# Performance work log

Hardware: AMD Instinct MI355X
Metric: run time of the kernel (lower is better)

## Reference

```python
import jax
import jax.numpy as jnp
from jax import lax
import numpy as np

DIM = 256
WIN = 7


def setup_inputs() -> dict:
    key = jax.random.key(0)
    ks = jax.random.split(key, 7)
    B, C, H, W = 16, DIM, 64, 64
    k = WIN
    return {
        "x": jax.random.normal(ks[0], (B, C, H, W), dtype=jnp.float32),
        "dw_weight": jax.random.normal(ks[1], (C, 1, k, k), dtype=jnp.float32) * 0.1,
        "pw_weight": jax.random.normal(ks[2], (C, C), dtype=jnp.float32) * 0.05,
        "w1": jax.random.normal(ks[3], (C // 4, C), dtype=jnp.float32) * 0.05,
        "b1": jax.random.normal(ks[4], (C // 4,), dtype=jnp.float32) * 0.05,
        "w2": jax.random.normal(ks[5], (C * k * k, C // 4), dtype=jnp.float32) * 0.05,
        "b2": jax.random.normal(ks[6], (C * k * k,), dtype=jnp.float32) * 0.05,
    }


def reference(x, dw_weight, pw_weight, w1, b1, w2, b2):
    B, C, H, W = x.shape
    k = dw_weight.shape[-1]
    pad = k // 2
    # dynamic kernel generator: global avg pool -> 1x1 conv -> GELU -> 1x1 conv
    pooled = x.mean(axis=(2, 3))                                  # [B, C]
    h = jax.nn.gelu(pooled @ w1.T + b1, approximate=False)        # [B, C//4]
    dyn = (h @ w2.T + b2).reshape(B, C, 1, k, k)                  # [B, C, 1, k, k]
    # fuse static depthwise weights with dynamic per-sample weights
    fused = dw_weight[None] + dyn                                  # [B, C, 1, k, k]
    # per-instance depthwise conv via groups = B*C
    x_flat = x.reshape(1, B * C, H, W)
    kern = fused.reshape(B * C, 1, k, k)
    out = lax.conv_general_dilated(
        x_flat, kern,
        window_strides=(1, 1),
        padding=[(pad, pad), (pad, pad)],
        feature_group_count=B * C,
        dimension_numbers=("NCHW", "OIHW", "NCHW"),
    )
    out = out.reshape(B, C, H, W)
    # final 1x1 pointwise conv (no bias)
    return jnp.einsum("bchw,oc->bohw", out, pw_weight)
```

## Files before the change

### kernel.cpp

```cpp
#include <hip/hip_runtime.h>
#include <math.h>
#include <stdint.h>

typedef __attribute__((ext_vector_type(8))) short short8;
typedef __attribute__((ext_vector_type(4))) float f32x4;

#define B_  16
#define C_  256
#define HW_ 4096
#define KK_ 49
#define CR_ 64

__device__ __forceinline__ ushort f2bf(float f) {
    union { float f; uint32_t u; } v; v.f = f;
    uint32_t r = (v.u + 0x7FFFu + ((v.u >> 16) & 1u)) >> 16;
    return (ushort)r;
}

__global__ __launch_bounds__(256) void pool_kernel(const float* __restrict__ x,
                                                   float* __restrict__ pooled) {
    int bc = blockIdx.x;
    const float4* p4 = (const float4*)(x + (size_t)bc * HW_);
    float s = 0.f;
    for (int i = threadIdx.x; i < HW_ / 4; i += 256) {
        float4 v = p4[i];
        s += (v.x + v.y) + (v.z + v.w);
    }
#pragma unroll
    for (int off = 32; off > 0; off >>= 1) s += __shfl_down(s, off);
    __shared__ float red[4];
    if ((threadIdx.x & 63) == 0) red[threadIdx.x >> 6] = s;
    __syncthreads();
    if (threadIdx.x == 0)
        pooled[bc] = (red[0] + red[1] + red[2] + red[3]) * (1.f / HW_);
}

__global__ __launch_bounds__(64) void mlp_kernel(const float* __restrict__ pooled,
                                                 const float* __restrict__ w1,
                                                 const float* __restrict__ b1,
                                                 float* __restrict__ h) {
    int b = blockIdx.x;
    int r = threadIdx.x;
    __shared__ float pr[C_];
    for (int i = r; i < C_; i += 64) pr[i] = pooled[b * C_ + i];
    __syncthreads();
    float acc = b1[r];
    const float* wr = w1 + (size_t)r * C_;
    for (int c = 0; c < C_; c += 4) {
        float4 wv = *(const float4*)(wr + c);
        acc += pr[c] * wv.x + pr[c + 1] * wv.y + pr[c + 2] * wv.z + pr[c + 3] * wv.w;
    }
    h[b * CR_ + r] = 0.5f * acc * (1.f + erff(acc * 0.70710678118654752f));
}

__global__ __launch_bounds__(256) void genw_kernel(const float* __restrict__ h,
                                                   const float* __restrict__ w2,
                                                   const float* __restrict__ b2,
                                                   const float* __restrict__ dw,
                                                   float* __restrict__ fused) {
    __shared__ float hs[B_ * CR_];
    int m = blockIdx.x * 256 + threadIdx.x;
    for (int i = threadIdx.x; i < B_ * CR_; i += 256) hs[i] = h[i];
    float wrow[CR_];
    const float4* w4 = (const float4*)(w2 + (size_t)m * CR_);
#pragma unroll
    for (int i = 0; i < CR_ / 4; i++) {
        float4 v = w4[i];
        wrow[4 * i] = v.x; wrow[4 * i + 1] = v.y;
        wrow[4 * i + 2] = v.z; wrow[4 * i + 3] = v.w;
    }
    float base = b2[m] + dw[m];
    __syncthreads();
    for (int b = 0; b < B_; b++) {
        float acc = base;
        const float* hb = hs + b * CR_;
#pragma unroll
        for (int r = 0; r < CR_; r++) acc += hb[r] * wrow[r];
        fused[(size_t)b * (C_ * KK_) + m] = acc;
    }
}

__global__ __launch_bounds__(256) void prep_kernel(const float* __restrict__ pw,
                                                   ushort* __restrict__ Pa) {
    int idx = blockIdx.x * 256 + threadIdx.x;
    int o = idx >> 8, c = idx & 255;
    Pa[(size_t)(((o >> 4) * 32) + (c >> 3)) * 128 + (o & 15) * 8 + (c & 7)] = f2bf(pw[idx]);
}

__global__ __launch_bounds__(512, 4) void dw_kernel(const float* __restrict__ x,
                                                    const float* __restrict__ fused,
                                                    ushort* __restrict__ Ug) {
    __shared__ __align__(16) float xs[8 * 22 * 72];
    ushort* Us = (ushort*)xs;

    const int strip = blockIdx.x;
    const int cb    = blockIdx.y;
    const int b     = blockIdx.z;
    const int tid   = threadIdx.x;
    const int wid   = tid >> 6;
    const int lane  = tid & 63;
    const int c0    = cb * 8;
    const int r0    = strip * 16;

    {
        const float* xp = x + (((size_t)(b * C_ + c0 + wid)) << 12);
        float* xd = xs + wid * 1584;
#pragma unroll
        for (int row = 0; row < 22; row++) {
            int gr = r0 + row - 3;
            float v = 0.f;
            if ((unsigned)gr < 64u) v = xp[(gr << 6) + lane];
            xd[row * 72 + 3 + lane] = v;
        }
        for (int j = lane; j < 176; j += 64) {
            int row = j >> 3, e = j & 7;
            int col = (e < 3) ? e : (64 + e);
            xd[row * 72 + col] = 0.f;
        }
    }

    float wk[49];
    {
        const float* fp = fused + (((size_t)b * C_) + c0 + wid) * KK_;
        float v = (lane < KK_) ? fp[lane] : 0.f;
        int vi = __float_as_int(v);
#pragma unroll
        for (int t = 0; t < 49; t++)
            wk[t] = __int_as_float(__builtin_amdgcn_readlane(vi, t));
    }
    __syncthreads();

    const int c = lane;
    float acc[16];
#pragma unroll
    for (int o = 0; o < 16; o++) acc[o] = 0.f;

    const float* xcol = xs + wid * 1584 + c;
#pragma unroll
    for (int ir = 0; ir < 22; ir++) {
        float x7[7];
#pragma unroll
        for (int j = 0; j < 7; j++) x7[j] = xcol[ir * 72 + j];
        const int olo = (ir - 6 < 0) ? 0 : ir - 6;
        const int ohi = (ir < 15) ? ir : 15;
#pragma unroll
        for (int o = olo; o <= ohi; o++) {
            const int ki = ir - o;
#pragma unroll
            for (int j = 0; j < 7; j++)
                acc[o] = fmaf(x7[j], wk[ki * 7 + j], acc[o]);
        }
    }
    __syncthreads();

#pragma unroll
    for (int o = 0; o < 16; o++)
        Us[(o * 4 + (c >> 4)) * 128 + (c & 15) * 8 + wid] = f2bf(acc[o]);
    __syncthreads();

    for (int t = tid; t < 1024; t += 512) {
        int q = t >> 4, part = t & 15;
        int o = q >> 2, cg = q & 3;
        size_t e = ((((size_t)b * 256) + (size_t)((r0 + o) * 4 + cg)) * 32 + cb) * 128
                   + (size_t)part * 8;
        *(uint4*)(Ug + e) = *(const uint4*)(Us + q * 128 + part * 8);
    }
}

#define GLDS16(gp, lp) __builtin_amdgcn_global_load_lds(\
    (const __attribute__((address_space(1))) uint32_t*)(gp), \
    (__attribute__((address_space(3))) uint32_t*)(lp), 16, 0, 0)

__global__ __launch_bounds__(256, 2) void pw_kernel(const ushort* __restrict__ Pa,
                                                    const ushort* __restrict__ Ug,
                                                    float* __restrict__ Y) {
    __shared__ ushort As[2][8192];
    __shared__ ushort Bs[2][4096];
    const int pb   = blockIdx.x;
    const int b    = blockIdx.y;
    const int tid  = threadIdx.x;
    const int w    = tid >> 6;
    const int lane = tid & 63;
    const int oi   = lane & 15;
    const int kq   = lane >> 4;

    f32x4 acc[4][8];
#pragma unroll
    for (int mi = 0; mi < 4; mi++)
#pragma unroll
        for (int ni = 0; ni < 8; ni++)
            acc[mi][ni] = (f32x4){0.f, 0.f, 0.f, 0.f};

    const size_t ubase = (((size_t)b * 256) + (size_t)pb * 8) * 32 * 128;

#define STAGE(BUF, KB0)                                                          \
    for (int q = w; q < 24; q += 4) {                                            \
        const ushort* src; ushort* dst;                                          \
        if (q < 16) { src = Pa + ((size_t)q * 32 + (KB0)) * 128;                 \
                      dst = &As[BUF][q * 512]; }                                 \
        else { int pg = q - 16;                                                  \
               src = Ug + ubase + ((size_t)pg * 32 + (KB0)) * 128;               \
               dst = &Bs[BUF][pg * 512]; }                                       \
        GLDS16(src + lane * 8, dst);                                             \
    }

    STAGE(0, 0)

#pragma unroll
    for (int ki = 0; ki < 8; ki++) {
        const int buf = ki & 1;
        if (ki < 7) {
            STAGE(buf ^ 1, (ki + 1) * 4)
            asm volatile("s_waitcnt vmcnt(6)" ::: "memory");
        } else {
            asm volatile("s_waitcnt vmcnt(0)" ::: "memory");
        }
        __builtin_amdgcn_s_barrier();
        __builtin_amdgcn_sched_barrier(0);

        short8 af[4], bf[8];
#pragma unroll
        for (int mi = 0; mi < 4; mi++)
            af[mi] = *(const short8*)&As[buf][(w * 4 + mi) * 512 + kq * 128 + oi * 8];
#pragma unroll
        for (int ni = 0; ni < 8; ni++)
            bf[ni] = *(const short8*)&Bs[buf][ni * 512 + kq * 128 + oi * 8];
#pragma unroll
        for (int mi = 0; mi < 4; mi++)
#pragma unroll
            for (int ni = 0; ni < 8; ni++)
                acc[mi][ni] = __builtin_amdgcn_mfma_f32_16x16x32_bf16(
                    af[mi], bf[ni], acc[mi][ni], 0, 0, 0);

        __builtin_amdgcn_s_barrier();
        __builtin_amdgcn_sched_barrier(0);
    }

    float* yb = Y + ((size_t)b << 20);
    const int p0 = pb * 128;
#pragma unroll
    for (int mi = 0; mi < 4; mi++) {
#pragma unroll
        for (int ni = 0; ni < 8; ni++) {
            int p = p0 + ni * 16 + oi;
#pragma unroll
            for (int r = 0; r < 4; r++) {
                int o = w * 64 + mi * 16 + kq * 4 + r;
                yb[(size_t)o * HW_ + p] = acc[mi][ni][r];
            }
        }
    }
#undef STAGE
}

extern "C" void kernel_launch(void* const* d_in, const int* in_sizes, int n_in,
                              void* d_out, int out_size, void* d_ws, size_t ws_size,
                              hipStream_t stream) {
    const float* x  = (const float*)d_in[0];
    const float* dw = (const float*)d_in[1];
    const float* pw = (const float*)d_in[2];
    const float* w1 = (const float*)d_in[3];
    const float* b1 = (const float*)d_in[4];
    const float* w2 = (const float*)d_in[5];
    const float* b2 = (const float*)d_in[6];
    float* out = (float*)d_out;

    char* ws = (char*)d_ws;
    float*  pooled = (float*)(ws);
    float*  h      = (float*)(ws + 16384);
    float*  fused  = (float*)(ws + 20480);
    ushort* Pa     = (ushort*)(ws + 823296);
    ushort* Ug     = (ushort*)(ws + 1048576);

    hipLaunchKernelGGL(pool_kernel, dim3(B_ * C_), dim3(256), 0, stream, x, pooled);
    hipLaunchKernelGGL(mlp_kernel,  dim3(B_), dim3(64), 0, stream, pooled, w1, b1, h);
    hipLaunchKernelGGL(genw_kernel, dim3(49), dim3(256), 0, stream, h, w2, b2, dw, fused);
    hipLaunchKernelGGL(prep_kernel, dim3(256), dim3(256), 0, stream, pw, Pa);
    hipLaunchKernelGGL(dw_kernel,   dim3(4, 32, B_), dim3(512), 0, stream, x, fused, Ug);
    hipLaunchKernelGGL(pw_kernel,   dim3(32, B_), dim3(256), 0, stream, Pa, Ug, out);
}
```

Baseline: 100.9 us.

## Register-tile depthwise conv as 4x4 output blocks with swizzled LDS staging

In the depthwise conv kernel, each lane now computes a 4-row by 4-column output tile instead of one column of 16 rows. Input rows are read with vector float4/float2 loads and reused across neighbouring columns, which cuts LDS reads per FMA. Weights are pinned to scalar registers with an asm constraint. The bf16 staging writes use an XOR swizzle, with the matching un-swizzle on readout, to avoid LDS bank conflicts. The wider loads and swizzle logic may raise register pressure or misalign accesses.

```diff
diff --git a/kernel.cpp b/kernel.cpp
--- a/kernel.cpp
+++ b/kernel.cpp
@@ -125,45 +125,62 @@
         float v = (lane < KK_) ? fp[lane] : 0.f;
         int vi = __float_as_int(v);
 #pragma unroll
-        for (int t = 0; t < 49; t++)
+        for (int t = 0; t < 49; t++) {
             wk[t] = __int_as_float(__builtin_amdgcn_readlane(vi, t));
-    }
-    __syncthreads();
-
-    const int c = lane;
-    float acc[16];
-#pragma unroll
-    for (int o = 0; o < 16; o++) acc[o] = 0.f;
-
-    const float* xcol = xs + wid * 1584 + c;
-#pragma unroll
-    for (int ir = 0; ir < 22; ir++) {
-        float x7[7];
-#pragma unroll
-        for (int j = 0; j < 7; j++) x7[j] = xcol[ir * 72 + j];
-        const int olo = (ir - 6 < 0) ? 0 : ir - 6;
-        const int ohi = (ir < 15) ? ir : 15;
-#pragma unroll
-        for (int o = olo; o <= ohi; o++) {
-            const int ki = ir - o;
-#pragma unroll
-            for (int j = 0; j < 7; j++)
-                acc[o] = fmaf(x7[j], wk[ki * 7 + j], acc[o]);
-        }
-    }
-    __syncthreads();
-
-#pragma unroll
-    for (int o = 0; o < 16; o++)
-        Us[(o * 4 + (c >> 4)) * 128 + (c & 15) * 8 + wid] = f2bf(acc[o]);
+            asm volatile("" : "+s"(wk[t]));
+        }
+    }
+    __syncthreads();
+
+    const int cg = lane & 15;
+    const int rg = lane >> 4;
+    float acc[4][4];
+#pragma unroll
+    for (int ro = 0; ro < 4; ro++)
+#pragma unroll
+        for (int co = 0; co < 4; co++) acc[ro][co] = 0.f;
+
+    const float* xbase = xs + wid * 1584 + (rg * 4) * 72 + cg * 4;
+#pragma unroll
+    for (int rr = 0; rr < 10; rr++) {
+        float xr[10];
+        *(float4*)&xr[0] = *(const float4*)(xbase + rr * 72);
+        *(float4*)&xr[4] = *(const float4*)(xbase + rr * 72 + 4);
+        *(float2*)&xr[8] = *(const float2*)(xbase + rr * 72 + 8);
+        const int olo = (rr - 6 < 0) ? 0 : rr - 6;
+        const int ohi = (rr < 3) ? rr : 3;
+#pragma unroll
+        for (int ro = olo; ro <= ohi; ro++) {
+            const int ki = rr - ro;
+#pragma unroll
+            for (int j = 0; j < 7; j++) {
+#pragma unroll
+                for (int co = 0; co < 4; co++)
+                    acc[ro][co] = fmaf(xr[co + j], wk[ki * 7 + j], acc[ro][co]);
+            }
+        }
+    }
+    __syncthreads();
+
+#pragma unroll
+    for (int ro = 0; ro < 4; ro++) {
+#pragma unroll
+        for (int co = 0; co < 4; co++) {
+            int o = rg * 4 + ro;
+            int c = cg * 4 + co;
+            int q = o * 4 + (c >> 4);
+            int part = (c & 15) ^ (q & 15);
+            Us[q * 128 + part * 8 + wid] = f2bf(acc[ro][co]);
+        }
+    }
     __syncthreads();
 
     for (int t = tid; t < 1024; t += 512) {
         int q = t >> 4, part = t & 15;
-        int o = q >> 2, cg = q & 3;
-        size_t e = ((((size_t)b * 256) + (size_t)((r0 + o) * 4 + cg)) * 32 + cb) * 128
+        int o = q >> 2, cgrp = q & 3;
+        size_t e = ((((size_t)b * 256) + (size_t)((r0 + o) * 4 + cgrp)) * 32 + cb) * 128
                    + (size_t)part * 8;
-        *(uint4*)(Ug + e) = *(const uint4*)(Us + q * 128 + part * 8);
+        *(uint4*)(Ug + e) = *(const uint4*)(Us + q * 128 + ((part ^ (q & 15)) * 8));
     }
 }
 
```

New measurement: 102.8 us. About the same (+1.8%).
